# Performance work log

Measured on AMD Instinct MI355X. Metric: run time of the kernel, lower is better.

## Reference

```python
import jax, jax.numpy as jnp
import numpy as np
import math

# dims (scaled-down DeepSeek-MLA-style config)
DIM = 2048
NH = 16
QLR = 768       # dla_q_lora_rank
KVLR = 512      # dla_kv_lora_rank
DN = 128        # qk_nope_head_dim
DR = 64         # qk_rope_head_dim
DV = 128        # v_head_dim
QKH = DN + DR   # 192
BSZ = 1
SEQ = 2048
LAYER_IDX = 3
LAMBDA_INIT = 0.8 - 0.6 * math.exp(-0.3 * LAYER_IDX)
SCALE = QKH ** -0.5  # max_seq_len == original_seq_len -> no mscale correction
MAX_SCORE = 100.0


def apply_rope(x, cos, sin):
    # x: [b, s, h, d]; consecutive pairs (x[2i], x[2i+1]) form complex numbers
    xr, xi = x[..., 0::2], x[..., 1::2]
    c = cos[None, :, None, :]
    sn = sin[None, :, None, :]
    yr = xr * c - xi * sn
    yi = xr * sn + xi * c
    return jnp.stack([yr, yi], axis=-1).reshape(x.shape)


def setup_inputs() -> dict:
    key = jax.random.key(0)
    ks = jax.random.split(key, 12)
    x = jax.random.normal(ks[0], (BSZ, SEQ, DIM), dtype=jnp.float32)
    s = 0.02
    wq_a = jax.random.normal(ks[1], (QLR, DIM), dtype=jnp.float32) * s
    wq_b = jax.random.normal(ks[2], (NH * QKH, QLR), dtype=jnp.float32) * s
    wkv_a = jax.random.normal(ks[3], (KVLR + DR, DIM), dtype=jnp.float32) * s
    wkv_b = jax.random.normal(ks[4], (NH * (DN + DV), KVLR), dtype=jnp.float32) * s
    wo = jax.random.normal(ks[5], (DIM, NH * DV), dtype=jnp.float32) * s
    lambda_q_nope = jax.random.normal(ks[6], (DN,), dtype=jnp.float32) * 0.1
    lambda_q_rope = jax.random.normal(ks[7], (DR,), dtype=jnp.float32) * 0.1
    lambda_k_nope = jax.random.normal(ks[8], (DN,), dtype=jnp.float32) * 0.1
    lambda_k_rope = jax.random.normal(ks[9], (DR,), dtype=jnp.float32) * 0.1
    # rope frequencies
    inv_freq = 1.0 / (10000.0 ** (np.arange(0, DR, 2, dtype=np.float32) / DR))
    angles = np.arange(SEQ, dtype=np.float32)[:, None] * inv_freq[None, :]
    freqs_cos = jnp.asarray(np.cos(angles))
    freqs_sin = jnp.asarray(np.sin(angles))
    # causal mask (prefill, start_pos = 0)
    mask = jnp.where(jnp.tril(jnp.ones((SEQ, SEQ), dtype=bool)), 0.0, -1e9).astype(jnp.float32)
    return {
        'x': x, 'wq_a': wq_a, 'wq_b': wq_b, 'wkv_a': wkv_a, 'wkv_b': wkv_b, 'wo': wo,
        'lambda_q_nope': lambda_q_nope, 'lambda_q_rope': lambda_q_rope,
        'lambda_k_nope': lambda_k_nope, 'lambda_k_rope': lambda_k_rope,
        'freqs_cos': freqs_cos, 'freqs_sin': freqs_sin, 'mask': mask, 'start_pos': 0,
    }


def reference(x, wq_a, wq_b, wkv_a, wkv_b, wo,
              lambda_q_nope, lambda_q_rope, lambda_k_nope, lambda_k_rope,
              freqs_cos, freqs_sin, mask, start_pos):
    b, s, _ = x.shape
    # differential-attention lambda scalar
    lam = (jnp.exp(jnp.dot(lambda_q_nope, lambda_k_nope))
           - jnp.exp(jnp.dot(lambda_q_rope, lambda_k_rope)) + LAMBDA_INIT)
    # low-rank q projection
    q = (x @ wq_a.T) @ wq_b.T                    # [b, s, NH*QKH]
    q = q.reshape(b, s, NH, QKH)
    q_nope, q_pe = q[..., :DN], q[..., DN:]
    q_pe = apply_rope(q_pe, freqs_cos, freqs_sin)
    # compressed kv + shared rope key
    kv_full = x @ wkv_a.T                        # [b, s, KVLR + DR]
    kv, k_pe = kv_full[..., :KVLR], kv_full[..., KVLR:]
    k_pe = apply_rope(k_pe[:, :, None, :], freqs_cos, freqs_sin)  # [b, s, 1, DR]
    kvb = (kv @ wkv_b.T).reshape(b, s, NH, DN + DV)
    k_nope, v = kvb[..., :DN], kvb[..., DN:]
    q_full = jnp.concatenate([q_nope, q_pe], axis=-1)             # [b, s, NH, 192]
    k_full = jnp.concatenate([k_nope, jnp.broadcast_to(k_pe, (b, s, NH, DR))], axis=-1)
    # differential split into two halves of qk_head_dim//2 = 96
    H = QKH // 2
    q1, q2 = q_full[..., :H], q_full[..., H:]
    k1, k2 = k_full[..., :H], k_full[..., H:]
    s1 = jnp.einsum('bshd,bthd->bhst', q1, k1) * SCALE
    s2 = jnp.einsum('bshd,bthd->bhst', q2, k2) * SCALE
    s1 = jnp.clip(s1, -MAX_SCORE, MAX_SCORE) + mask[None, None]
    s2 = jnp.clip(s2, -MAX_SCORE, MAX_SCORE) + mask[None, None]
    attn = jax.nn.softmax(s1, axis=-1) - lam * jax.nn.softmax(s2, axis=-1)
    out = jnp.einsum('bhst,bthd->bshd', attn, v)  # [b, s, NH, DV]
    out = out * (1.0 - LAMBDA_INIT)
    return out.reshape(b, s, NH * DV) @ wo.T
```

## Files before the change

kernel.cpp:

```cpp
#include <hip/hip_runtime.h>
#include <stdint.h>

#define SEQ   2048
#define NH    16
#define DIMM  2048
#define QLR   768
#define KVLR  512
#define DN    128
#define DR    64
#define DV    128
#define QKH   192
#define KVPAD 640
#define SCALE_F 0.07216878364870323f
#define LAM_INIT 0.5560582f
#define C1F      0.4439418f
#define PSTR  36
#define DTHR  8.0f

typedef __attribute__((ext_vector_type(8))) uint16_t u16x8;
typedef __attribute__((ext_vector_type(8))) __bf16   bf16x8;
typedef __attribute__((ext_vector_type(4))) float    f32x4;

#define MFMA16(a,b,c) __builtin_amdgcn_mfma_f32_16x16x32_bf16((a),(b),(c),0,0,0)

__device__ __forceinline__ uint16_t f2bf(float f){ uint32_t x; __builtin_memcpy(&x,&f,4); return (uint16_t)((x + 0x7FFFu + ((x>>16)&1u))>>16); }
__device__ __forceinline__ bf16x8 ldfrag(const uint16_t* p){ return __builtin_bit_cast(bf16x8, *(const u16x8*)p); }
__device__ __forceinline__ void gload_lds16(const uint16_t* g, uint16_t* l){
  __builtin_amdgcn_global_load_lds((const __attribute__((address_space(1))) void*)g,
                                   (__attribute__((address_space(3))) void*)l, 16, 0, 0);
}
__device__ __forceinline__ void stor(uint16_t* p, float v){ *p = f2bf(v); }
__device__ __forceinline__ void stor(float* p, float v){ *p = v; }

__global__ void cvt(const float* __restrict__ in, uint16_t* __restrict__ outp){
  int i = (blockIdx.x*256 + threadIdx.x)*8;
  float4 a = *(const float4*)(in + i);
  float4 b = *(const float4*)(in + i + 4);
  u16x8 r;
  r[0]=f2bf(a.x); r[1]=f2bf(a.y); r[2]=f2bf(a.z); r[3]=f2bf(a.w);
  r[4]=f2bf(b.x); r[5]=f2bf(b.y); r[6]=f2bf(b.z); r[7]=f2bf(b.w);
  *(u16x8*)(outp + i) = r;
}

__global__ void pad_wkva(const float* __restrict__ in, uint16_t* __restrict__ outp){
  int idx = blockIdx.x*256 + threadIdx.x;
  int n = idx >> 11;
  outp[idx] = (n < 576) ? f2bf(in[idx]) : (uint16_t)0;
}

template <typename OT>
__global__ __launch_bounds__(256) void gemm_bt(const uint16_t* __restrict__ A, int lda,
                                               const uint16_t* __restrict__ B,
                                               OT* __restrict__ C, int ldc, int K)
{
  __shared__ __align__(16) uint16_t As[128*32];
  __shared__ __align__(16) uint16_t Bs[128*32];
  const int tid  = threadIdx.x;
  const int wid  = tid >> 6;
  const int lane = tid & 63;
  const int wr   = (wid >> 1) * 64;
  const int wc   = (wid & 1) * 64;
  const int srow = lane >> 2;
  const int scol = (lane & 3) * 8;
  const uint16_t* Abase = A + (size_t)(blockIdx.x * 128) * lda;
  const uint16_t* Bbase = B + (size_t)(blockIdx.y * 128) * K;
  f32x4 acc[4][4] = {};
  for (int k0 = 0; k0 < K; k0 += 32) {
    __syncthreads();
#pragma unroll
    for (int c = 0; c < 2; ++c) {
      int r = (wid*2 + c)*16 + srow;
      gload_lds16(Abase + (size_t)r*lda + k0 + scol, &As[(wid*2 + c)*512]);
      gload_lds16(Bbase + (size_t)r*K   + k0 + scol, &Bs[(wid*2 + c)*512]);
    }
    __syncthreads();
    bf16x8 af[4], bfr[4];
#pragma unroll
    for (int m = 0; m < 4; ++m)
      af[m] = ldfrag(&As[(wr + m*16 + (lane&15))*32 + ((lane>>4)*8)]);
#pragma unroll
    for (int n = 0; n < 4; ++n)
      bfr[n] = ldfrag(&Bs[(wc + n*16 + (lane&15))*32 + ((lane>>4)*8)]);
#pragma unroll
    for (int m = 0; m < 4; ++m)
#pragma unroll
      for (int n = 0; n < 4; ++n)
        acc[m][n] = MFMA16(af[m], bfr[n], acc[m][n]);
  }
  const int rbase = blockIdx.x*128 + wr + ((lane>>4)<<2);
  const int cbase = blockIdx.y*128 + wc + (lane&15);
#pragma unroll
  for (int m = 0; m < 4; ++m)
#pragma unroll
    for (int n = 0; n < 4; ++n)
#pragma unroll
      for (int r = 0; r < 4; ++r)
        stor(&C[(size_t)(rbase + m*16 + r)*ldc + cbase + n*16], acc[m][n][r]);
}

__global__ void lam_kernel(const float* lqn, const float* lqr,
                           const float* lkn, const float* lkr, float* outp){
  if (threadIdx.x == 0 && blockIdx.x == 0) {
    float d1 = 0.f, d2 = 0.f;
    for (int i = 0; i < DN; ++i) d1 += lqn[i] * lkn[i];
    for (int i = 0; i < DR; ++i) d2 += lqr[i] * lkr[i];
    outp[0] = __expf(d1) - __expf(d2) + LAM_INIT;
  }
}

__global__ void rope_q(uint16_t* __restrict__ q, const float* __restrict__ cs,
                       const float* __restrict__ sn){
  int idx = blockIdx.x*256 + threadIdx.x;
  int j = idx & 31, hh = (idx>>5) & 15, s = idx >> 9;
  uint16_t* p = q + (size_t)s*(NH*QKH) + hh*QKH + DN + 2*j;
  float xr = (float)__builtin_bit_cast(__bf16, p[0]);
  float xi = (float)__builtin_bit_cast(__bf16, p[1]);
  float c = cs[s*32+j], si = sn[s*32+j];
  p[0] = f2bf(xr*c - xi*si);
  p[1] = f2bf(xr*si + xi*c);
}

__global__ void mat_k(const uint16_t* __restrict__ kvb, const uint16_t* __restrict__ kvf,
                      const float* __restrict__ cs, const float* __restrict__ sn,
                      uint16_t* __restrict__ kfull){
  int idx = blockIdx.x*256 + threadIdx.x;
  int d = idx % QKH; int th = idx / QKH; int t = th & 2047; int hh = th >> 11;
  uint16_t val;
  if (d < DN) {
    val = kvb[(size_t)t*4096 + hh*256 + d];
  } else {
    int dd = d - DN, j = dd >> 1;
    float xr = (float)__builtin_bit_cast(__bf16, kvf[(size_t)t*KVPAD + KVLR + 2*j]);
    float xi = (float)__builtin_bit_cast(__bf16, kvf[(size_t)t*KVPAD + KVLR + 2*j + 1]);
    float c = cs[t*32+j], si = sn[t*32+j];
    val = f2bf((dd & 1) ? (xr*si + xi*c) : (xr*c - xi*si));
  }
  kfull[idx] = val;
}

__global__ void mat_v(const uint16_t* __restrict__ kvb, uint16_t* __restrict__ vtp){
  int idx = blockIdx.x*256 + threadIdx.x;
  int t = idx & 2047, d = (idx>>11) & 127, hh = idx >> 18;
  vtp[idx] = kvb[(size_t)t*4096 + hh*256 + DN + d];
}

__global__ __launch_bounds__(64) __attribute__((amdgpu_waves_per_eu(2)))
void attn_kernel(
    const uint16_t* __restrict__ q,
    const uint16_t* __restrict__ kf,
    const uint16_t* __restrict__ vt,
    const float* __restrict__ lamp,
    uint16_t* __restrict__ o)
{
  __shared__ __align__(16) uint16_t P_lds[4][16*PSTR];
  const int b  = blockIdx.x;
  const int h  = b & 15;
  const int c  = b >> 4;
  const int lane = threadIdx.x & 63;
  const int l15 = lane & 15;
  const int lhi = lane >> 4;
  const int subrow = lhi * 4;
  const int qrow0 = c * 16;
  const int kend  = qrow0 + 16;
  const float lam = lamp[0];

  bf16x8 qf[6];
  {
    const uint16_t* qbase = q + (size_t)(qrow0 + l15)*(NH*QKH) + h*QKH + lhi*8;
#pragma unroll
    for (int kb = 0; kb < 6; ++kb) qf[kb] = ldfrag(qbase + kb*32);
  }
  f32x4 O1[8] = {}, O2[8] = {};
  float m1[4], m2[4], l1[4], l2[4];
#pragma unroll
  for (int r = 0; r < 4; ++r) { m1[r] = m2[r] = -1e30f; l1[r] = l2[r] = 0.f; }

  const uint16_t* kbase = kf + (size_t)h*SEQ*QKH;
  const uint16_t* vbase = vt + (size_t)h*DV*SEQ;

  auto loadK = [&](bf16x8 (&k0)[6], bf16x8 (&k1)[6], int t0){
    const uint16_t* kp0 = kbase + (size_t)(t0 + l15)*QKH + lhi*8;
    const uint16_t* kp1 = kp0 + (size_t)16*QKH;
#pragma unroll
    for (int kb = 0; kb < 6; ++kb) { k0[kb] = ldfrag(kp0 + kb*32); k1[kb] = ldfrag(kp1 + kb*32); }
  };
  auto loadV = [&](bf16x8 (&vf)[8], int t0){
#pragma unroll
    for (int n = 0; n < 8; ++n) vf[n] = ldfrag(vbase + (size_t)(n*16 + l15)*SEQ + t0 + lhi*8);
  };
  auto qk = [&](bf16x8 (&k0)[6], bf16x8 (&k1)[6], f32x4 (&s1)[2], f32x4 (&s2)[2]){
    __builtin_amdgcn_s_setprio(1);
#pragma unroll
    for (int kb = 0; kb < 3; ++kb) { s1[0] = MFMA16(qf[kb], k0[kb], s1[0]); s1[1] = MFMA16(qf[kb], k1[kb], s1[1]); }
#pragma unroll
    for (int kb = 3; kb < 6; ++kb) { s2[0] = MFMA16(qf[kb], k0[kb], s2[0]); s2[1] = MFMA16(qf[kb], k1[kb], s2[1]); }
    __builtin_amdgcn_s_setprio(0);
  };
  auto smax = [&](f32x4 (&s1)[2], f32x4 (&s2)[2], int t0, bool MASKED,
                  uint16_t* pa, uint16_t* pb){
#pragma unroll
    for (int half = 0; half < 2; ++half)
#pragma unroll
      for (int r = 0; r < 4; ++r) {
        float v1 = fminf(fmaxf(s1[half][r]*SCALE_F, -100.f), 100.f);
        float v2 = fminf(fmaxf(s2[half][r]*SCALE_F, -100.f), 100.f);
        if (MASKED && (t0 + half*16 + l15 > qrow0 + subrow + r)) { v1 = -1e30f; v2 = -1e30f; }
        s1[half][r] = v1; s2[half][r] = v2;
      }
    float t1[4], t2[4];
#pragma unroll
    for (int r = 0; r < 4; ++r) { t1[r] = fmaxf(s1[0][r], s1[1][r]); t2[r] = fmaxf(s2[0][r], s2[1][r]); }
#pragma unroll
    for (int off = 1; off < 16; off <<= 1)
#pragma unroll
      for (int r = 0; r < 4; ++r) {
        t1[r] = fmaxf(t1[r], __shfl_xor(t1[r], off, 64));
        t2[r] = fmaxf(t2[r], __shfl_xor(t2[r], off, 64));
      }
    bool ok1 = (t1[0] <= m1[0]+DTHR) && (t1[1] <= m1[1]+DTHR) && (t1[2] <= m1[2]+DTHR) && (t1[3] <= m1[3]+DTHR);
    if (!__all(ok1)) {
#pragma unroll
      for (int r = 0; r < 4; ++r) {
        float mn = fmaxf(m1[r], t1[r]);
        float cr = __expf(m1[r] - mn);
        m1[r] = mn; l1[r] *= cr;
#pragma unroll
        for (int n = 0; n < 8; ++n) O1[n][r] *= cr;
      }
    }
    bool ok2 = (t2[0] <= m2[0]+DTHR) && (t2[1] <= m2[1]+DTHR) && (t2[2] <= m2[2]+DTHR) && (t2[3] <= m2[3]+DTHR);
    if (!__all(ok2)) {
#pragma unroll
      for (int r = 0; r < 4; ++r) {
        float mn = fmaxf(m2[r], t2[r]);
        float cr = __expf(m2[r] - mn);
        m2[r] = mn; l2[r] *= cr;
#pragma unroll
        for (int n = 0; n < 8; ++n) O2[n][r] *= cr;
      }
    }
    float rs1[4], rs2[4];
#pragma unroll
    for (int r = 0; r < 4; ++r) {
      float p10 = __expf(s1[0][r] - m1[r]), p11 = __expf(s1[1][r] - m1[r]);
      float p20 = __expf(s2[0][r] - m2[r]), p21 = __expf(s2[1][r] - m2[r]);
      pa[(subrow + r)*PSTR +      l15] = f2bf(p10);
      pa[(subrow + r)*PSTR + 16 + l15] = f2bf(p11);
      pb[(subrow + r)*PSTR +      l15] = f2bf(p20);
      pb[(subrow + r)*PSTR + 16 + l15] = f2bf(p21);
      rs1[r] = p10 + p11; rs2[r] = p20 + p21;
    }
#pragma unroll
    for (int off = 1; off < 16; off <<= 1)
#pragma unroll
      for (int r = 0; r < 4; ++r) {
        rs1[r] += __shfl_xor(rs1[r], off, 64);
        rs2[r] += __shfl_xor(rs2[r], off, 64);
      }
#pragma unroll
    for (int r = 0; r < 4; ++r) { l1[r] += rs1[r]; l2[r] += rs2[r]; }
  };
  auto pv = [&](bf16x8 (&vf)[8], const uint16_t* pa, const uint16_t* pb){
    bf16x8 pf0 = ldfrag(&pa[l15*PSTR + lhi*8]);
    bf16x8 pf1 = ldfrag(&pb[l15*PSTR + lhi*8]);
    __builtin_amdgcn_s_setprio(1);
#pragma unroll
    for (int n = 0; n < 8; ++n) {
      O1[n] = MFMA16(pf0, vf[n], O1[n]);
      O2[n] = MFMA16(pf1, vf[n], O2[n]);
    }
    __builtin_amdgcn_s_setprio(0);
  };

  uint16_t* plA0 = &P_lds[0][0]; uint16_t* plA1 = &P_lds[1][0];
  uint16_t* plB0 = &P_lds[2][0]; uint16_t* plB1 = &P_lds[3][0];

  const int n_tiles = (kend + 31) >> 5;
  const int n_unm   = n_tiles - 1;
  const int n_pairs = n_unm >> 1;

  bf16x8 kr0[6], kr1[6], vfa[8], vfb[8];
  int t0 = 0;
  for (int p = 0; p < n_pairs; ++p, t0 += 64) {
    const int ta = t0, tb = t0 + 32;
    loadK(kr0, kr1, ta);
    loadV(vfa, ta);
    f32x4 sA1[2] = {}, sA2[2] = {};
    qk(kr0, kr1, sA1, sA2);
    loadK(kr0, kr1, tb);
    smax(sA1, sA2, ta, false, plA0, plA1);
    f32x4 sB1[2] = {}, sB2[2] = {};
    qk(kr0, kr1, sB1, sB2);
    loadV(vfb, tb);
    smax(sB1, sB2, tb, false, plB0, plB1);
    asm volatile("s_waitcnt lgkmcnt(0)" ::: "memory");
    __builtin_amdgcn_sched_barrier(0);
    pv(vfa, plA0, plA1);
    pv(vfb, plB0, plB1);
  }
  if (n_unm & 1) {
    loadK(kr0, kr1, t0);
    loadV(vfa, t0);
    f32x4 s1[2] = {}, s2[2] = {};
    qk(kr0, kr1, s1, s2);
    smax(s1, s2, t0, false, plA0, plA1);
    asm volatile("s_waitcnt lgkmcnt(0)" ::: "memory");
    __builtin_amdgcn_sched_barrier(0);
    pv(vfa, plA0, plA1);
    t0 += 32;
  }
  {
    loadK(kr0, kr1, t0);
    loadV(vfa, t0);
    f32x4 s1[2] = {}, s2[2] = {};
    qk(kr0, kr1, s1, s2);
    smax(s1, s2, t0, true, plA0, plA1);
    asm volatile("s_waitcnt lgkmcnt(0)" ::: "memory");
    __builtin_amdgcn_sched_barrier(0);
    pv(vfa, plA0, plA1);
  }

#pragma unroll
  for (int r = 0; r < 4; ++r) {
    float inv1 = 1.f / l1[r], inv2 = lam / l2[r];
#pragma unroll
    for (int n = 0; n < 8; ++n) {
      float val = (O1[n][r]*inv1 - O2[n][r]*inv2) * C1F;
      o[(size_t)(qrow0 + subrow + r)*(NH*DV) + h*DV + n*16 + l15] = f2bf(val);
    }
  }
}

extern "C" void kernel_launch(void* const* d_in, const int* in_sizes, int n_in,
                              void* d_out, int out_size, void* d_ws, size_t ws_size,
                              hipStream_t stream)
{
  const float* x     = (const float*)d_in[0];
  const float* wq_a  = (const float*)d_in[1];
  const float* wq_b  = (const float*)d_in[2];
  const float* wkv_a = (const float*)d_in[3];
  const float* wkv_b = (const float*)d_in[4];
  const float* wo    = (const float*)d_in[5];
  const float* lqn   = (const float*)d_in[6];
  const float* lqr   = (const float*)d_in[7];
  const float* lkn   = (const float*)d_in[8];
  const float* lkr   = (const float*)d_in[9];
  const float* fcos  = (const float*)d_in[10];
  const float* fsin  = (const float*)d_in[11];

  char* ws = (char*)d_ws;
  size_t off = 0;
  float*    lam    = (float*)(ws + off);  off += 256;
  uint16_t* xb     = (uint16_t*)(ws + off); off += (size_t)DIMM*DIMM*2;
  uint16_t* wqab   = (uint16_t*)(ws + off); off += (size_t)QLR*DIMM*2;
  uint16_t* wqbb   = (uint16_t*)(ws + off); off += (size_t)NH*QKH*QLR*2;
  uint16_t* wkvap  = (uint16_t*)(ws + off); off += (size_t)KVPAD*DIMM*2;
  uint16_t* wkvbb  = (uint16_t*)(ws + off); off += (size_t)4096*KVLR*2;
  uint16_t* wob    = (uint16_t*)(ws + off); off += (size_t)DIMM*DIMM*2;
  uint16_t* qlat   = (uint16_t*)(ws + off); off += (size_t)SEQ*QLR*2;
  uint16_t* qbuf   = (uint16_t*)(ws + off); off += (size_t)SEQ*NH*QKH*2;
  uint16_t* kvfull = (uint16_t*)(ws + off); off += (size_t)SEQ*KVPAD*2;
  uint16_t* kvb    = (uint16_t*)(ws + off); off += (size_t)SEQ*4096*2;
  uint16_t* kfull  = (uint16_t*)(ws + off); off += (size_t)NH*SEQ*QKH*2;
  uint16_t* vtb    = (uint16_t*)(ws + off); off += (size_t)NH*DV*SEQ*2;
  uint16_t* attn   = (uint16_t*)(ws + off); off += (size_t)SEQ*NH*DV*2;

  lam_kernel<<<1, 64, 0, stream>>>(lqn, lqr, lkn, lkr, lam);
  cvt<<<2048, 256, 0, stream>>>(x, xb);
  cvt<<< 768, 256, 0, stream>>>(wq_a, wqab);
  cvt<<<1152, 256, 0, stream>>>(wq_b, wqbb);
  cvt<<<1024, 256, 0, stream>>>(wkv_b, wkvbb);
  cvt<<<2048, 256, 0, stream>>>(wo, wob);
  pad_wkva<<<5120, 256, 0, stream>>>(wkv_a, wkvap);

  gemm_bt<<<dim3(16, 6), 256, 0, stream>>>(xb, DIMM, wqab, qlat, QLR, DIMM);
  gemm_bt<<<dim3(16, 24), 256, 0, stream>>>(qlat, QLR, wqbb, qbuf, NH*QKH, QLR);
  rope_q<<<4096, 256, 0, stream>>>(qbuf, fcos, fsin);
  gemm_bt<<<dim3(16, 5), 256, 0, stream>>>(xb, DIMM, wkvap, kvfull, KVPAD, DIMM);
  gemm_bt<<<dim3(16, 32), 256, 0, stream>>>(kvfull, KVPAD, wkvbb, kvb, 4096, KVLR);
  mat_k<<<24576, 256, 0, stream>>>(kvb, kvfull, fcos, fsin, kfull);
  mat_v<<<16384, 256, 0, stream>>>(kvb, vtb);
  attn_kernel<<<2048, 64, 0, stream>>>(qbuf, kfull, vtb, lam, attn);
  gemm_bt<<<dim3(16, 16), 256, 0, stream>>>(attn, NH*DV, wob, (float*)d_out, DIMM, DIMM);
}
```

Measured before the change: 414.6 us.

## Fuse kv_b GEMM epilogue into K/V layouts and split attention keys across four waves

```diff
diff --git a/kernel.cpp b/kernel.cpp
--- a/kernel.cpp
+++ b/kernel.cpp
@@ -24,6 +24,7 @@
 #define MFMA16(a,b,c) __builtin_amdgcn_mfma_f32_16x16x32_bf16((a),(b),(c),0,0,0)
 
 __device__ __forceinline__ uint16_t f2bf(float f){ uint32_t x; __builtin_memcpy(&x,&f,4); return (uint16_t)((x + 0x7FFFu + ((x>>16)&1u))>>16); }
+__device__ __forceinline__ float bfu(uint16_t u){ return (float)__builtin_bit_cast(__bf16, u); }
 __device__ __forceinline__ bf16x8 ldfrag(const uint16_t* p){ return __builtin_bit_cast(bf16x8, *(const u16x8*)p); }
 __device__ __forceinline__ void gload_lds16(const uint16_t* g, uint16_t* l){
   __builtin_amdgcn_global_load_lds((const __attribute__((address_space(1))) void*)g,
@@ -98,6 +99,62 @@
         stor(&C[(size_t)(rbase + m*16 + r)*ldc + cbase + n*16], acc[m][n][r]);
 }
 
+__global__ __launch_bounds__(256) void gemm_kvb(const uint16_t* __restrict__ A, int lda,
+                                                const uint16_t* __restrict__ B,
+                                                uint16_t* __restrict__ kfull,
+                                                uint16_t* __restrict__ vtb, int K)
+{
+  __shared__ __align__(16) uint16_t As[128*32];
+  __shared__ __align__(16) uint16_t Bs[128*32];
+  const int tid  = threadIdx.x;
+  const int wid  = tid >> 6;
+  const int lane = tid & 63;
+  const int wr   = (wid >> 1) * 64;
+  const int wc   = (wid & 1) * 64;
+  const int srow = lane >> 2;
+  const int scol = (lane & 3) * 8;
+  const uint16_t* Abase = A + (size_t)(blockIdx.x * 128) * lda;
+  const uint16_t* Bbase = B + (size_t)(blockIdx.y * 128) * K;
+  f32x4 acc[4][4] = {};
+  for (int k0 = 0; k0 < K; k0 += 32) {
+    __syncthreads();
+#pragma unroll
+    for (int c = 0; c < 2; ++c) {
+      int r = (wid*2 + c)*16 + srow;
+      gload_lds16(Abase + (size_t)r*lda + k0 + scol, &As[(wid*2 + c)*512]);
+      gload_lds16(Bbase + (size_t)r*K   + k0 + scol, &Bs[(wid*2 + c)*512]);
+    }
+    __syncthreads();
+    bf16x8 af[4], bfr[4];
+#pragma unroll
+    for (int m = 0; m < 4; ++m)
+      af[m] = ldfrag(&As[(wr + m*16 + (lane&15))*32 + ((lane>>4)*8)]);
+#pragma unroll
+    for (int n = 0; n < 4; ++n)
+      bfr[n] = ldfrag(&Bs[(wc + n*16 + (lane&15))*32 + ((lane>>4)*8)]);
+#pragma unroll
+    for (int m = 0; m < 4; ++m)
+#pragma unroll
+      for (int n = 0; n < 4; ++n)
+        acc[m][n] = MFMA16(af[m], bfr[n], acc[m][n]);
+  }
+  const int rbase = blockIdx.x*128 + wr + ((lane>>4)<<2);
+  const int cbase = blockIdx.y*128 + wc + (lane&15);
+#pragma unroll
+  for (int m = 0; m < 4; ++m)
+#pragma unroll
+    for (int n = 0; n < 4; ++n) {
+      const int gcol = cbase + n*16;
+      const int hh = gcol >> 8, d = gcol & 255;
+#pragma unroll
+      for (int r = 0; r < 4; ++r) {
+        const int t = rbase + m*16 + r;
+        if (d < DN) kfull[((size_t)hh*SEQ + t)*QKH + d] = f2bf(acc[m][n][r]);
+        else        vtb[((size_t)hh*DV + (d - DN))*SEQ + t] = f2bf(acc[m][n][r]);
+      }
+    }
+}
+
 __global__ void lam_kernel(const float* lqn, const float* lqr,
                            const float* lkn, const float* lkr, float* outp){
   if (threadIdx.x == 0 && blockIdx.x == 0) {
@@ -113,38 +170,25 @@
   int idx = blockIdx.x*256 + threadIdx.x;
   int j = idx & 31, hh = (idx>>5) & 15, s = idx >> 9;
   uint16_t* p = q + (size_t)s*(NH*QKH) + hh*QKH + DN + 2*j;
-  float xr = (float)__builtin_bit_cast(__bf16, p[0]);
-  float xi = (float)__builtin_bit_cast(__bf16, p[1]);
+  float xr = bfu(p[0]), xi = bfu(p[1]);
   float c = cs[s*32+j], si = sn[s*32+j];
   p[0] = f2bf(xr*c - xi*si);
   p[1] = f2bf(xr*si + xi*c);
 }
 
-__global__ void mat_k(const uint16_t* __restrict__ kvb, const uint16_t* __restrict__ kvf,
-                      const float* __restrict__ cs, const float* __restrict__ sn,
-                      uint16_t* __restrict__ kfull){
+__global__ void rope_k(const uint16_t* __restrict__ kvf, const float* __restrict__ cs,
+                       const float* __restrict__ sn, uint16_t* __restrict__ kfull){
   int idx = blockIdx.x*256 + threadIdx.x;
-  int d = idx % QKH; int th = idx / QKH; int t = th & 2047; int hh = th >> 11;
-  uint16_t val;
-  if (d < DN) {
-    val = kvb[(size_t)t*4096 + hh*256 + d];
-  } else {
-    int dd = d - DN, j = dd >> 1;
-    float xr = (float)__builtin_bit_cast(__bf16, kvf[(size_t)t*KVPAD + KVLR + 2*j]);
-    float xi = (float)__builtin_bit_cast(__bf16, kvf[(size_t)t*KVPAD + KVLR + 2*j + 1]);
-    float c = cs[t*32+j], si = sn[t*32+j];
-    val = f2bf((dd & 1) ? (xr*si + xi*c) : (xr*c - xi*si));
-  }
-  kfull[idx] = val;
-}
-
-__global__ void mat_v(const uint16_t* __restrict__ kvb, uint16_t* __restrict__ vtp){
-  int idx = blockIdx.x*256 + threadIdx.x;
-  int t = idx & 2047, d = (idx>>11) & 127, hh = idx >> 18;
-  vtp[idx] = kvb[(size_t)t*4096 + hh*256 + DN + d];
-}
-
-__global__ __launch_bounds__(64) __attribute__((amdgpu_waves_per_eu(2)))
+  int j = idx & 31, t = (idx>>5) & 2047, hh = idx >> 16;
+  float xr = bfu(kvf[(size_t)t*KVPAD + KVLR + 2*j]);
+  float xi = bfu(kvf[(size_t)t*KVPAD + KVLR + 2*j + 1]);
+  float c = cs[t*32+j], si = sn[t*32+j];
+  uint16_t* p = kfull + ((size_t)hh*SEQ + t)*QKH + DN + 2*j;
+  p[0] = f2bf(xr*c - xi*si);
+  p[1] = f2bf(xr*si + xi*c);
+}
+
+__global__ __launch_bounds__(256) __attribute__((amdgpu_waves_per_eu(4)))
 void attn_kernel(
     const uint16_t* __restrict__ q,
     const uint16_t* __restrict__ kf,
@@ -152,10 +196,12 @@
     const float* __restrict__ lamp,
     uint16_t* __restrict__ o)
 {
-  __shared__ __align__(16) uint16_t P_lds[4][16*PSTR];
+  __shared__ __align__(16) uint16_t P_lds[4][4][16*PSTR];
+  __shared__ float R_lds[2][64*41];
   const int b  = blockIdx.x;
   const int h  = b & 15;
   const int c  = b >> 4;
+  const int wid  = threadIdx.x >> 6;
   const int lane = threadIdx.x & 63;
   const int l15 = lane & 15;
   const int lhi = lane >> 4;
@@ -272,17 +318,16 @@
     __builtin_amdgcn_s_setprio(0);
   };
 
-  uint16_t* plA0 = &P_lds[0][0]; uint16_t* plA1 = &P_lds[1][0];
-  uint16_t* plB0 = &P_lds[2][0]; uint16_t* plB1 = &P_lds[3][0];
+  uint16_t* plA0 = &P_lds[wid][0][0]; uint16_t* plA1 = &P_lds[wid][1][0];
+  uint16_t* plB0 = &P_lds[wid][2][0]; uint16_t* plB1 = &P_lds[wid][3][0];
 
   const int n_tiles = (kend + 31) >> 5;
-  const int n_unm   = n_tiles - 1;
-  const int n_pairs = n_unm >> 1;
+  const int nm = n_tiles - 1;
 
   bf16x8 kr0[6], kr1[6], vfa[8], vfb[8];
-  int t0 = 0;
-  for (int p = 0; p < n_pairs; ++p, t0 += 64) {
-    const int ta = t0, tb = t0 + 32;
+  int i = wid;
+  for (; i + 4 < nm; i += 8) {
+    const int ta = i*32, tb = (i+4)*32;
     loadK(kr0, kr1, ta);
     loadV(vfa, ta);
     f32x4 sA1[2] = {}, sA2[2] = {};
@@ -298,35 +343,73 @@
     pv(vfa, plA0, plA1);
     pv(vfb, plB0, plB1);
   }
-  if (n_unm & 1) {
-    loadK(kr0, kr1, t0);
-    loadV(vfa, t0);
+  if (i < nm) {
+    loadK(kr0, kr1, i*32);
+    loadV(vfa, i*32);
     f32x4 s1[2] = {}, s2[2] = {};
     qk(kr0, kr1, s1, s2);
-    smax(s1, s2, t0, false, plA0, plA1);
+    smax(s1, s2, i*32, false, plA0, plA1);
     asm volatile("s_waitcnt lgkmcnt(0)" ::: "memory");
     __builtin_amdgcn_sched_barrier(0);
     pv(vfa, plA0, plA1);
-    t0 += 32;
-  }
-  {
-    loadK(kr0, kr1, t0);
-    loadV(vfa, t0);
+  }
+  if ((nm & 3) == wid) {
+    loadK(kr0, kr1, nm*32);
+    loadV(vfa, nm*32);
     f32x4 s1[2] = {}, s2[2] = {};
     qk(kr0, kr1, s1, s2);
-    smax(s1, s2, t0, true, plA0, plA1);
+    smax(s1, s2, nm*32, true, plA0, plA1);
     asm volatile("s_waitcnt lgkmcnt(0)" ::: "memory");
     __builtin_amdgcn_sched_barrier(0);
     pv(vfa, plA0, plA1);
   }
 
-#pragma unroll
-  for (int r = 0; r < 4; ++r) {
-    float inv1 = 1.f / l1[r], inv2 = lam / l2[r];
-#pragma unroll
-    for (int n = 0; n < 8; ++n) {
-      float val = (O1[n][r]*inv1 - O2[n][r]*inv2) * C1F;
-      o[(size_t)(qrow0 + subrow + r)*(NH*DV) + h*DV + n*16 + l15] = f2bf(val);
+  auto write_state = [&](float* buf, const float* mm, const float* ll, const f32x4* O){
+    float* p = buf + lane*41;
+#pragma unroll
+    for (int r = 0; r < 4; ++r) { p[r] = mm[r]; p[4+r] = ll[r]; }
+#pragma unroll
+    for (int n = 0; n < 8; ++n)
+#pragma unroll
+      for (int r = 0; r < 4; ++r) p[8 + n*4 + r] = O[n][r];
+  };
+  auto merge_state = [&](const float* buf, float* mm, float* ll, f32x4* O){
+    const float* p = buf + lane*41;
+    float ca[4], cb[4];
+#pragma unroll
+    for (int r = 0; r < 4; ++r) {
+      float mo = p[r], lo = p[4+r];
+      float mn = fmaxf(mm[r], mo);
+      ca[r] = __expf(mm[r] - mn); cb[r] = __expf(mo - mn);
+      mm[r] = mn; ll[r] = ll[r]*ca[r] + lo*cb[r];
+    }
+#pragma unroll
+    for (int n = 0; n < 8; ++n)
+#pragma unroll
+      for (int r = 0; r < 4; ++r) O[n][r] = O[n][r]*ca[r] + p[8 + n*4 + r]*cb[r];
+  };
+
+  if (wid >= 2) write_state(R_lds[wid-2], m1, l1, O1);
+  __syncthreads();
+  if (wid < 2)  merge_state(R_lds[wid], m1, l1, O1);
+  __syncthreads();
+  if (wid >= 2) write_state(R_lds[wid-2], m2, l2, O2);
+  __syncthreads();
+  if (wid < 2)  merge_state(R_lds[wid], m2, l2, O2);
+  __syncthreads();
+  if (wid == 1) { write_state(R_lds[0], m1, l1, O1); write_state(R_lds[1], m2, l2, O2); }
+  __syncthreads();
+  if (wid == 0) {
+    merge_state(R_lds[0], m1, l1, O1);
+    merge_state(R_lds[1], m2, l2, O2);
+#pragma unroll
+    for (int r = 0; r < 4; ++r) {
+      float inv1 = 1.f / l1[r], inv2 = lam / l2[r];
+#pragma unroll
+      for (int n = 0; n < 8; ++n) {
+        float val = (O1[n][r]*inv1 - O2[n][r]*inv2) * C1F;
+        o[(size_t)(qrow0 + subrow + r)*(NH*DV) + h*DV + n*16 + l15] = f2bf(val);
+      }
     }
   }
 }
@@ -360,7 +443,6 @@
   uint16_t* qlat   = (uint16_t*)(ws + off); off += (size_t)SEQ*QLR*2;
   uint16_t* qbuf   = (uint16_t*)(ws + off); off += (size_t)SEQ*NH*QKH*2;
   uint16_t* kvfull = (uint16_t*)(ws + off); off += (size_t)SEQ*KVPAD*2;
-  uint16_t* kvb    = (uint16_t*)(ws + off); off += (size_t)SEQ*4096*2;
   uint16_t* kfull  = (uint16_t*)(ws + off); off += (size_t)NH*SEQ*QKH*2;
   uint16_t* vtb    = (uint16_t*)(ws + off); off += (size_t)NH*DV*SEQ*2;
   uint16_t* attn   = (uint16_t*)(ws + off); off += (size_t)SEQ*NH*DV*2;
@@ -377,9 +459,8 @@
   gemm_bt<<<dim3(16, 24), 256, 0, stream>>>(qlat, QLR, wqbb, qbuf, NH*QKH, QLR);
   rope_q<<<4096, 256, 0, stream>>>(qbuf, fcos, fsin);
   gemm_bt<<<dim3(16, 5), 256, 0, stream>>>(xb, DIMM, wkvap, kvfull, KVPAD, DIMM);
-  gemm_bt<<<dim3(16, 32), 256, 0, stream>>>(kvfull, KVPAD, wkvbb, kvb, 4096, KVLR);
-  mat_k<<<24576, 256, 0, stream>>>(kvb, kvfull, fcos, fsin, kfull);
-  mat_v<<<16384, 256, 0, stream>>>(kvb, vtb);
-  attn_kernel<<<2048, 64, 0, stream>>>(qbuf, kfull, vtb, lam, attn);
+  gemm_kvb<<<dim3(16, 32), 256, 0, stream>>>(kvfull, KVPAD, wkvbb, kfull, vtb, KVLR);
+  rope_k<<<4096, 256, 0, stream>>>(kvfull, fcos, fsin, kfull);
+  attn_kernel<<<2048, 256, 0, stream>>>(qbuf, kfull, vtb, lam, attn);
   gemm_bt<<<dim3(16, 16), 256, 0, stream>>>(attn, NH*DV, wob, (float*)d_out, DIMM, DIMM);
 }
```

New measurement: 730.3 us. 76.2% more time.
